# Kernel optimization log

Hardware: AMD Instinct MI355X
Metric: run time of the kernel (lower is better)

Reference implementation:

```python
import jax, jax.numpy as jnp
import numpy as np
import math

EMBED_DIM = 1024
MEMORY_DIM = 1024
MEMORY_SIZE = 2048
B, S = 8, 4096


def bitnet_linear(x, W, b):
    """Eval-mode BitNetLinear: 1.58-bit weight quant + 8-bit activation quant."""
    w_scale = jnp.mean(jnp.abs(W))
    qW = jnp.sign(W) * (jnp.abs(W) > 0.5 * w_scale).astype(W.dtype)
    i_scale = jnp.max(jnp.abs(x)) / 127.0
    qx = jnp.clip(jnp.round(x / i_scale), -128.0, 127.0)
    out = jnp.einsum('bsi,oi->bso', qx, qW) * (w_scale * i_scale)
    return out + b


def setup_inputs() -> dict:
    key = jax.random.key(0)
    ks = jax.random.split(key, 9)
    return {
        'x': jax.random.normal(ks[0], (B, S, EMBED_DIM), jnp.float32),
        'memory_keys': jax.random.normal(ks[1], (MEMORY_SIZE, MEMORY_DIM), jnp.float32),
        'memory_values': jax.random.normal(ks[2], (MEMORY_SIZE, EMBED_DIM), jnp.float32),
        'Wk': jax.random.normal(ks[3], (MEMORY_DIM, EMBED_DIM), jnp.float32) * 0.1,
        'bk': jnp.zeros((MEMORY_DIM,), jnp.float32),
        'Wv': jax.random.normal(ks[4], (EMBED_DIM, EMBED_DIM), jnp.float32) * 0.1,
        'bv': jnp.zeros((EMBED_DIM,), jnp.float32),
        'Wo': jax.random.normal(ks[5], (EMBED_DIM, EMBED_DIM), jnp.float32) * 0.1,
        'bo': jnp.zeros((EMBED_DIM,), jnp.float32),
    }


def reference(x, memory_keys, memory_values, Wk, bk, Wv, bv, Wo, bo):
    # quantized key/value projections
    query_keys = bitnet_linear(x, Wk, bk)          # [B, S, Dm]
    _query_values = bitnet_linear(x, Wv, bv)       # computed in original (used only by update path)
    # memory cross-attention over fixed bank
    similarities = jnp.einsum('bsd,md->bsm', query_keys, memory_keys)  # [B, S, M]
    attention_weights = jax.nn.softmax(similarities / math.sqrt(MEMORY_DIM), axis=-1)
    retrieved = jnp.einsum('bsm,me->bse', attention_weights, memory_values)  # [B, S, E]
    output = bitnet_linear(x + retrieved, Wo, bo)
    return output
```

## Files before the change

### kernel.cpp

```cpp
#include <hip/hip_runtime.h>
#include <hip/hip_bf16.h>
#include <stdint.h>
#include <type_traits>

typedef __attribute__((ext_vector_type(8))) short bf16x8;
typedef __attribute__((ext_vector_type(4))) int i32x4;
typedef __attribute__((ext_vector_type(16))) float f32x16;
typedef __attribute__((ext_vector_type(16))) int i32x16;

struct Scalars {
  double sum_wk;
  double sum_wo;
  unsigned int max_x_bits;
  unsigned int max_y_bits;
};

__device__ __forceinline__ unsigned short f2bf(float f) {
  __hip_bfloat16 h = __float2bfloat16(f);
  return *reinterpret_cast<unsigned short*>(&h);
}

__device__ __forceinline__ void async16(void* lds, const void* g) {
  __builtin_amdgcn_global_load_lds((__attribute__((address_space(1))) void*)g,
                                   (__attribute__((address_space(3))) void*)lds, 16, 0, 0);
}

__device__ __forceinline__ void tile_swizzle(int nxShift, int& bx, int& by) {
  const int per = gridDim.x >> 3;
  const int tile = (blockIdx.x & 7) * per + (blockIdx.x >> 3);
  bx = tile & ((1 << nxShift) - 1);
  by = tile >> nxShift;
}

__device__ __forceinline__ f32x16 mm32(bf16x8 a, bf16x8 b, f32x16 c) {
  return __builtin_amdgcn_mfma_f32_32x32x16_bf16(a, b, c, 0, 0, 0);
}
__device__ __forceinline__ i32x16 mm32(i32x4 a, i32x4 b, i32x16 c) {
  return __builtin_amdgcn_mfma_i32_32x32x32_i8(a, b, c, 0, 0, 0);
}

__global__ __launch_bounds__(256) void stats_kernel(const float* __restrict__ Wk,
                                                    const float* __restrict__ Wo,
                                                    const float* __restrict__ x,
                                                    Scalars* __restrict__ sc) {
  const int which = blockIdx.y;
  size_t tid = (size_t)blockIdx.x * 256 + threadIdx.x;
  size_t stride = (size_t)gridDim.x * 256;
  if (which < 2) {
    const float* w = which ? Wo : Wk;
    const size_t n = 1048576;
    double s = 0.0;
    for (size_t i = tid * 4; i < n; i += stride * 4) {
      float4 v = *(const float4*)(w + i);
      s += (double)fabsf(v.x) + (double)fabsf(v.y) + (double)fabsf(v.z) + (double)fabsf(v.w);
    }
#pragma unroll
    for (int o = 32; o > 0; o >>= 1) s += __shfl_xor(s, o);
    __shared__ double sm[4];
    if ((threadIdx.x & 63) == 0) sm[threadIdx.x >> 6] = s;
    __syncthreads();
    if (threadIdx.x == 0)
      atomicAdd(which ? &sc->sum_wo : &sc->sum_wk, sm[0] + sm[1] + sm[2] + sm[3]);
  } else {
    const size_t n = (size_t)32768 * 1024;
    float m = 0.0f;
    for (size_t i = tid * 4; i < n; i += stride * 4) {
      float4 v = *(const float4*)(x + i);
      m = fmaxf(m, fmaxf(fmaxf(fabsf(v.x), fabsf(v.y)), fmaxf(fabsf(v.z), fabsf(v.w))));
    }
#pragma unroll
    for (int o = 32; o > 0; o >>= 1) m = fmaxf(m, __shfl_xor(m, o));
    __shared__ float smf[4];
    if ((threadIdx.x & 63) == 0) smf[threadIdx.x >> 6] = m;
    __syncthreads();
    if (threadIdx.x == 0)
      atomicMax(&sc->max_x_bits,
                __float_as_uint(fmaxf(fmaxf(smf[0], smf[1]), fmaxf(smf[2], smf[3]))));
  }
}

__global__ __launch_bounds__(256) void prep_kernel(
    const float* __restrict__ Wk, const float* __restrict__ Wo,
    const float* __restrict__ mk, const float* __restrict__ mv,
    const float* __restrict__ x, char* __restrict__ qWk8, char* __restrict__ qWo8,
    __hip_bfloat16* __restrict__ mkb, __hip_bfloat16* __restrict__ mvT,
    char* __restrict__ qx8, const Scalars* __restrict__ sc) {
  __shared__ float tl[32][33];
  const int which = blockIdx.y;
  const int t = threadIdx.x;
  size_t tid = (size_t)blockIdx.x * 256 + t;
  size_t stride = (size_t)gridDim.x * 256;
  if (which < 2) {
    const float* W = which ? Wo : Wk;
    char* q = which ? qWo8 : qWk8;
    const double sum = which ? sc->sum_wo : sc->sum_wk;
    const float thr = 0.5f * (float)(sum * (1.0 / 1048576.0));
    const size_t n = 1048576;
    for (size_t i = tid * 4; i < n; i += stride * 4) {
      float4 v = *(const float4*)(W + i);
      char4 o;
      o.x = (char)(fabsf(v.x) > thr ? (v.x > 0.f ? 1 : -1) : 0);
      o.y = (char)(fabsf(v.y) > thr ? (v.y > 0.f ? 1 : -1) : 0);
      o.z = (char)(fabsf(v.z) > thr ? (v.z > 0.f ? 1 : -1) : 0);
      o.w = (char)(fabsf(v.w) > thr ? (v.w > 0.f ? 1 : -1) : 0);
      *(char4*)(q + i) = o;
    }
  } else if (which == 2) {
    const size_t n = (size_t)2048 * 1024;
    for (size_t i = tid * 4; i < n; i += stride * 4) {
      float4 v = *(const float4*)(mk + i);
      ushort4 o;
      o.x = f2bf(v.x); o.y = f2bf(v.y); o.z = f2bf(v.z); o.w = f2bf(v.w);
      *(ushort4*)((unsigned short*)mkb + i) = o;
    }
  } else if (which == 3) {
    const int ti = blockIdx.x & 31;
    const int tj = blockIdx.x >> 5;
    const int tx = t & 31, ty = t >> 5;
#pragma unroll
    for (int r = 0; r < 4; ++r)
      tl[ty + r * 8][tx] = mv[(size_t)(tj * 32 + ty + r * 8) * 1024 + ti * 32 + tx];
    __syncthreads();
#pragma unroll
    for (int r = 0; r < 4; ++r)
      mvT[(size_t)(ti * 32 + ty + r * 8) * 2048 + tj * 32 + tx] =
          __float2bfloat16(tl[tx][ty + r * 8]);
  } else {
    const float isc = __uint_as_float(sc->max_x_bits) / 127.0f;
    const size_t n = (size_t)32768 * 1024;
    for (size_t i = tid * 4; i < n; i += stride * 4) {
      float4 v = *(const float4*)(x + i);
      char4 o;
      o.x = (char)(int)fminf(fmaxf(rintf(v.x / isc), -128.f), 127.f);
      o.y = (char)(int)fminf(fmaxf(rintf(v.y / isc), -128.f), 127.f);
      o.z = (char)(int)fminf(fmaxf(rintf(v.z / isc), -128.f), 127.f);
      o.w = (char)(int)fminf(fmaxf(rintf(v.w / isc), -128.f), 127.f);
      *(char4*)(qx8 + i) = o;
    }
  }
}

__global__ __launch_bounds__(256) void quant_act_i8_kernel(const float* __restrict__ x,
                                                           char* __restrict__ q,
                                                           const unsigned int* __restrict__ maxbits,
                                                           size_t n) {
  const float isc = __uint_as_float(*maxbits) / 127.0f;
  size_t tid = (size_t)blockIdx.x * blockDim.x + threadIdx.x;
  size_t stride = (size_t)gridDim.x * blockDim.x;
  for (size_t i = tid * 4; i < n; i += stride * 4) {
    float4 v = *(const float4*)(x + i);
    char4 o;
    o.x = (char)(int)fminf(fmaxf(rintf(v.x / isc), -128.f), 127.f);
    o.y = (char)(int)fminf(fmaxf(rintf(v.y / isc), -128.f), 127.f);
    o.z = (char)(int)fminf(fmaxf(rintf(v.z / isc), -128.f), 127.f);
    o.w = (char)(int)fminf(fmaxf(rintf(v.w / isc), -128.f), 127.f);
    *(char4*)(q + i) = o;
  }
}

__global__ __launch_bounds__(256) void softmax_kernel(__hip_bfloat16* __restrict__ sims) {
  unsigned short* row = (unsigned short*)(sims + (size_t)blockIdx.x * 2048);
  const int t = threadIdx.x;
  const int l = t & 63, wv = t >> 6;
  uint4 r4 = *(const uint4*)(row + t * 8);
  float v[8];
  v[0] = __uint_as_float(r4.x << 16); v[1] = __uint_as_float(r4.x & 0xffff0000u);
  v[2] = __uint_as_float(r4.y << 16); v[3] = __uint_as_float(r4.y & 0xffff0000u);
  v[4] = __uint_as_float(r4.z << 16); v[5] = __uint_as_float(r4.z & 0xffff0000u);
  v[6] = __uint_as_float(r4.w << 16); v[7] = __uint_as_float(r4.w & 0xffff0000u);
  float m = v[0];
#pragma unroll
  for (int i = 1; i < 8; ++i) m = fmaxf(m, v[i]);
#pragma unroll
  for (int o = 32; o > 0; o >>= 1) m = fmaxf(m, __shfl_xor(m, o));
  __shared__ float red[4], red2[4];
  if (l == 0) red[wv] = m;
  __syncthreads();
  m = fmaxf(fmaxf(red[0], red[1]), fmaxf(red[2], red[3]));
  float s = 0.f;
#pragma unroll
  for (int i = 0; i < 8; ++i) { v[i] = expf(v[i] - m); s += v[i]; }
#pragma unroll
  for (int o = 32; o > 0; o >>= 1) s += __shfl_xor(s, o);
  if (l == 0) red2[wv] = s;
  __syncthreads();
  s = red2[0] + red2[1] + red2[2] + red2[3];
  unsigned short b[8];
#pragma unroll
  for (int i = 0; i < 8; ++i) b[i] = f2bf(v[i] / s);
  uint4 o4;
  o4.x = (unsigned)b[0] | ((unsigned)b[1] << 16);
  o4.y = (unsigned)b[2] | ((unsigned)b[3] << 16);
  o4.z = (unsigned)b[4] | ((unsigned)b[5] << 16);
  o4.w = (unsigned)b[6] | ((unsigned)b[7] << 16);
  *(uint4*)(row + t * 8) = o4;
}

#define CFENCE() asm volatile("" ::: "memory")
#define BAR8() { CFENCE(); __builtin_amdgcn_s_barrier(); CFENCE(); }
#define WLGKM(N) { asm volatile("s_waitcnt lgkmcnt(" #N ")" ::: "memory"); __builtin_amdgcn_sched_barrier(0); }
#define WVM(N) asm volatile("s_waitcnt vmcnt(" #N ")" ::: "memory")

template <int EPI>
__global__ __launch_bounds__(512, 2) void gemm8(
    const char* __restrict__ A, const char* __restrict__ B, void* __restrict__ C,
    const float* __restrict__ aux, Scalars* __restrict__ sc,
    int Ndim, int KB, int nxShift) {
  constexpr bool I8 = (EPI >= 3);
  using FR  = typename std::conditional<I8, i32x4, bf16x8>::type;
  using ACC = typename std::conditional<I8, i32x16, f32x16>::type;
  __shared__ __align__(16) char lds[4][2][16384];

  int bx, by;
  tile_swizzle(nxShift, bx, by);
  const int rowBlk = by * 256, colBlk = bx * 256;

  const int t = threadIdx.x, w = t >> 6, l = t & 63;
  const int wm = w >> 2, wn = w & 3;
  const int l31 = l & 31, hi = l >> 5;
  const int NT = KB >> 7, NIT = NT >> 1;

  int voA[2][2], voB[2][2];
#pragma unroll
  for (int hf = 0; hf < 2; ++hf)
#pragma unroll
    for (int j = 0; j < 2; ++j) {
      const int idx = j * 64 + (t >> 3);
      const int kby = ((t & 7) ^ (idx & 7)) << 4;
      voA[hf][j] = (rowBlk + ((idx >> 6) << 7) + (hf << 6) + (idx & 63)) * KB + kby;
      voB[hf][j] = (colBlk + ((idx >> 5) << 6) + (hf << 5) + (idx & 31)) * KB + kby;
    }

  int ofsK[4];
#pragma unroll
  for (int ks = 0; ks < 4; ++ks)
    ofsK[ks] = ((((ks ^ ((l >> 1) & 3)) << 1) | (hi ^ (l & 1))) << 4);
  const char* bA = &lds[0][0][0] + (wm * 64 + l31) * 128;
  const char* bB = &lds[2][0][0] + (wn * 32 + l31) * 128;

#define STG_A(slot, hf, tk)                                                         \
  if ((tk) < NT) {                                                                  \
    _Pragma("unroll") for (int j = 0; j < 2; ++j)                                   \
      async16(&lds[hf][slot][j * 8192 + (w << 10)],                                 \
              A + (((size_t)(tk)) << 7) + voA[hf][j]);                              \
  }
#define STG_B(slot, hf, tk)                                                         \
  if ((tk) < NT) {                                                                  \
    _Pragma("unroll") for (int j = 0; j < 2; ++j)                                   \
      async16(&lds[2 + (hf)][slot][j * 8192 + (w << 10)],                           \
              B + (((size_t)(tk)) << 7) + voB[hf][j]);                              \
  }

#define LD_A(dst, slot, hf, f01, ks) \
  dst = *(const FR*)(bA + ((hf) * 32768 + (slot) * 16384 + (f01) * 4096) + ofsK[ks]);
#define LD_B(dst, slot, nh, ks) \
  dst = *(const FR*)(bB + ((nh) * 32768 + (slot) * 16384) + ofsK[ks]);

#define R_A0(s) { _Pragma("unroll") for (int f_ = 0; f_ < 2; ++f_) _Pragma("unroll") for (int k_ = 0; k_ < 4; ++k_) LD_A(af[f_][k_], s, 0, f_, k_); }
#define R_A1(s) { _Pragma("unroll") for (int f_ = 0; f_ < 2; ++f_) _Pragma("unroll") for (int k_ = 0; k_ < 4; ++k_) LD_A(af[f_][k_], s, 1, f_, k_); }
#define R_B0(s) { _Pragma("unroll") for (int k_ = 0; k_ < 4; ++k_) LD_B(b0[k_], s, 0, k_); }
#define R_B1(s) { _Pragma("unroll") for (int k_ = 0; k_ < 4; ++k_) LD_B(b1[k_], s, 1, k_); }

#define MM32(MH, NH, BR)                                                            \
  __builtin_amdgcn_s_setprio(1);                                                    \
  _Pragma("unroll") for (int k_ = 0; k_ < 4; ++k_)                                  \
    _Pragma("unroll") for (int f_ = 0; f_ < 2; ++f_)                                \
      acc[(MH) * 2 + f_][NH] = mm32(af[f_][k_], BR[k_], acc[(MH) * 2 + f_][NH]);    \
  __builtin_amdgcn_s_setprio(0);

#define TSTEP(s, tk, last)                                                          \
  {                                                                                 \
                     \
    R_B1(s);                                                                        \
    STG_A((s) ^ 1, 1, (tk) + 1);                                                    \
    BAR8(); WLGKM(4);                                                               \
    MM32(0, 0, b0);                                                                 \
    BAR8();                                                                         \
        \
    STG_A(s, 0, (tk) + 2);                                                          \
    BAR8(); WLGKM(0);                                                               \
    MM32(0, 1, b1);                                                                 \
    R_A1(s);                                                                        \
    BAR8();                                                                         \
                                                                \
    STG_B(s, 0, (tk) + 2);                                                          \
    BAR8(); WLGKM(0);                                                               \
    MM32(1, 0, b0);                                                                 \
    BAR8();                                                                         \
           \
    STG_B(s, 1, (tk) + 2);                                                          \
    if (last) { WVM(0); } else { WVM(6); }                                          \
    BAR8();                                                                         \
    MM32(1, 1, b1);                                                                 \
    R_A0((s) ^ 1); R_B0((s) ^ 1);                                                   \
  }

  FR af[2][4], b0[4], b1[4];
  ACC acc[4][2] = {};

  STG_A(0, 0, 0); STG_B(0, 0, 0); STG_B(0, 1, 0); STG_A(0, 1, 0);
  CFENCE();
  STG_A(1, 0, 1); STG_B(1, 0, 1); STG_B(1, 1, 1);
  WVM(6);
  BAR8();
  R_A0(0); R_B0(0);

  for (int it = 0; it < NIT; ++it) {
    const bool last = (it == NIT - 1);
    TSTEP(0, it * 2, last);
    TSTEP(1, it * 2 + 1, last);
  }

  float sK = 0.0f;
  if constexpr (EPI == 3)
    sK = (float)(sc->sum_wk * (1.0 / 1048576.0)) * (__uint_as_float(sc->max_x_bits) / 127.0f);
  if constexpr (EPI == 4)
    sK = (float)(sc->sum_wo * (1.0 / 1048576.0)) * (__uint_as_float(sc->max_y_bits) / 127.0f);

  float amax = 0.0f;
#pragma unroll
  for (int f = 0; f < 4; ++f) {
#pragma unroll
    for (int g = 0; g < 2; ++g) {
      const int col = colBlk + wn * 64 + g * 32 + l31;
#pragma unroll
      for (int r = 0; r < 16; ++r) {
        const int row = rowBlk + wm * 128 + f * 32 + (r & 3) + 8 * (r >> 2) + 4 * hi;
        if constexpr (EPI == 1) {
          ((__hip_bfloat16*)C)[(size_t)row * Ndim + col] =
              __float2bfloat16(acc[f][g][r] * 0.03125f);
        } else if constexpr (EPI == 2) {
          float v = acc[f][g][r] + aux[(size_t)row * Ndim + col];
          ((float*)C)[(size_t)row * Ndim + col] = v;
          amax = fmaxf(amax, fabsf(v));
        } else if constexpr (EPI == 3) {
          ((__hip_bfloat16*)C)[(size_t)row * Ndim + col] =
              __float2bfloat16((float)acc[f][g][r] * sK + aux[col]);
        } else {
          ((float*)C)[(size_t)row * Ndim + col] = (float)acc[f][g][r] * sK + aux[col];
        }
      }
    }
  }

  if constexpr (EPI == 2) {
    __shared__ float wred[8];
#pragma unroll
    for (int o = 32; o > 0; o >>= 1) amax = fmaxf(amax, __shfl_xor(amax, o));
    if (l == 0) wred[w] = amax;
    __syncthreads();
    if (t == 0) {
      float m = wred[0];
#pragma unroll
      for (int i = 1; i < 8; ++i) m = fmaxf(m, wred[i]);
      atomicMax(&sc->max_y_bits, __float_as_uint(m));
    }
  }
#undef STG_A
#undef STG_B
#undef LD_A
#undef LD_B
#undef R_A0
#undef R_A1
#undef R_B0
#undef R_B1
#undef MM32
#undef TSTEP
}

extern "C" void kernel_launch(void* const* d_in, const int* in_sizes, int n_in,
                              void* d_out, int out_size, void* d_ws, size_t ws_size,
                              hipStream_t stream) {
  (void)in_sizes; (void)n_in; (void)out_size; (void)ws_size;
  const float* x  = (const float*)d_in[0];
  const float* mk = (const float*)d_in[1];
  const float* mv = (const float*)d_in[2];
  const float* Wk = (const float*)d_in[3];
  const float* bk = (const float*)d_in[4];
  const float* Wo = (const float*)d_in[7];
  const float* bo = (const float*)d_in[8];
  float* out = (float*)d_out;

  const int M = 32768, E = 1024, MEM = 2048;

  char* ws = (char*)d_ws;
  Scalars* sc = (Scalars*)ws;
  const size_t off0 = 256;
  char* qx8 = ws + off0;
  __hip_bfloat16* qk = (__hip_bfloat16*)(ws + off0 + (size_t)M * E);
  float* y = (float*)(ws + off0);
  const size_t off1 = off0 + (size_t)M * E * 4;
  __hip_bfloat16* sims = (__hip_bfloat16*)(ws + off1);
  char* qy8 = (char*)sims;
  const size_t off2 = off1 + (size_t)M * MEM * 2;
  char* qWk8 = ws + off2;
  char* qWo8 = qWk8 + (size_t)E * E;
  __hip_bfloat16* mkb = (__hip_bfloat16*)(qWo8 + (size_t)E * E);
  __hip_bfloat16* mvT = mkb + (size_t)MEM * E;

  hipMemsetAsync(ws, 0, 256, stream);

  stats_kernel<<<dim3(1024, 3), dim3(256), 0, stream>>>(Wk, Wo, x, sc);
  prep_kernel<<<dim3(2048, 5), dim3(256), 0, stream>>>(Wk, Wo, mk, mv, x, qWk8, qWo8,
                                                       mkb, mvT, qx8, sc);

  gemm8<3><<<dim3((E / 256) * (M / 256)), dim3(512), 0, stream>>>(
      qx8, qWk8, qk, bk, sc, E, E, 2);
  gemm8<1><<<dim3((MEM / 256) * (M / 256)), dim3(512), 0, stream>>>(
      (const char*)qk, (const char*)mkb, sims, nullptr, sc, MEM, 2 * E, 3);
  softmax_kernel<<<dim3(M), dim3(256), 0, stream>>>(sims);
  gemm8<2><<<dim3((E / 256) * (M / 256)), dim3(512), 0, stream>>>(
      (const char*)sims, (const char*)mvT, y, x, sc, E, 2 * MEM, 2);
  quant_act_i8_kernel<<<dim3(2048), dim3(256), 0, stream>>>(y, qy8, &sc->max_y_bits, (size_t)M * E);
  gemm8<4><<<dim3((E / 256) * (M / 256)), dim3(512), 0, stream>>>(
      qy8, qWo8, out, bo, sc, E, E, 2);
}
```

Baseline: 738.0 us.

## Switch GEMM inner loop from 32x32 to 16x16 MFMA tiles

Replaces the 32x32x16 bf16 and 32x32x32 i8 MFMA instructions with the 16x16x32 bf16 and 16x16x64 i8 variants. The LDS fragment addressing, the swizzle, the register fragment layout and the epilogue row/column mapping are all rebuilt for 16x16 tiles. The explicit lgkmcnt waits are removed, so the compiler now inserts the LDS waits. The per-block amax reduction through shared memory is replaced by one atomicMax per wave. This risks different LDS read patterns and scheduling, and makes more atomics per block.

```diff
diff --git a/kernel.cpp b/kernel.cpp
--- a/kernel.cpp
+++ b/kernel.cpp
@@ -4,9 +4,8 @@
 #include <type_traits>
 
 typedef __attribute__((ext_vector_type(8))) short bf16x8;
+typedef __attribute__((ext_vector_type(4))) float f32x4;
 typedef __attribute__((ext_vector_type(4))) int i32x4;
-typedef __attribute__((ext_vector_type(16))) float f32x16;
-typedef __attribute__((ext_vector_type(16))) int i32x16;
 
 struct Scalars {
   double sum_wk;
@@ -32,11 +31,11 @@
   by = tile >> nxShift;
 }
 
-__device__ __forceinline__ f32x16 mm32(bf16x8 a, bf16x8 b, f32x16 c) {
-  return __builtin_amdgcn_mfma_f32_32x32x16_bf16(a, b, c, 0, 0, 0);
-}
-__device__ __forceinline__ i32x16 mm32(i32x4 a, i32x4 b, i32x16 c) {
-  return __builtin_amdgcn_mfma_i32_32x32x32_i8(a, b, c, 0, 0, 0);
+__device__ __forceinline__ f32x4 mm(bf16x8 a, bf16x8 b, f32x4 c) {
+  return __builtin_amdgcn_mfma_f32_16x16x32_bf16(a, b, c, 0, 0, 0);
+}
+__device__ __forceinline__ i32x4 mm(i32x4 a, i32x4 b, i32x4 c) {
+  return __builtin_amdgcn_mfma_i32_16x16x64_i8(a, b, c, 0, 0, 0);
 }
 
 __global__ __launch_bounds__(256) void stats_kernel(const float* __restrict__ Wk,
@@ -198,7 +197,6 @@
 
 #define CFENCE() asm volatile("" ::: "memory")
 #define BAR8() { CFENCE(); __builtin_amdgcn_s_barrier(); CFENCE(); }
-#define WLGKM(N) { asm volatile("s_waitcnt lgkmcnt(" #N ")" ::: "memory"); __builtin_amdgcn_sched_barrier(0); }
 #define WVM(N) asm volatile("s_waitcnt vmcnt(" #N ")" ::: "memory")
 
 template <int EPI>
@@ -208,7 +206,7 @@
     int Ndim, int KB, int nxShift) {
   constexpr bool I8 = (EPI >= 3);
   using FR  = typename std::conditional<I8, i32x4, bf16x8>::type;
-  using ACC = typename std::conditional<I8, i32x16, f32x16>::type;
+  using ACC = typename std::conditional<I8, i32x4, f32x4>::type;
   __shared__ __align__(16) char lds[4][2][16384];
 
   int bx, by;
@@ -217,7 +215,7 @@
 
   const int t = threadIdx.x, w = t >> 6, l = t & 63;
   const int wm = w >> 2, wn = w & 3;
-  const int l31 = l & 31, hi = l >> 5;
+  const int quad = l >> 4, m16 = l & 15;
   const int NT = KB >> 7, NIT = NT >> 1;
 
   int voA[2][2], voB[2][2];
@@ -231,12 +229,14 @@
       voB[hf][j] = (colBlk + ((idx >> 5) << 6) + (hf << 5) + (idx & 31)) * KB + kby;
     }
 
-  int ofsK[4];
-#pragma unroll
-  for (int ks = 0; ks < 4; ++ks)
-    ofsK[ks] = ((((ks ^ ((l >> 1) & 3)) << 1) | (hi ^ (l & 1))) << 4);
-  const char* bA = &lds[0][0][0] + (wm * 64 + l31) * 128;
-  const char* bB = &lds[2][0][0] + (wn * 32 + l31) * 128;
+  const char* baA[2];
+  const char* baB[2];
+#pragma unroll
+  for (int ks = 0; ks < 2; ++ks) {
+    const int x16 = ((ks << 6) + (quad << 4)) ^ ((m16 & 7) << 4);
+    baA[ks] = &lds[0][0][(wm * 64 + m16) * 128 + x16];
+    baB[ks] = &lds[2][0][(wn * 32 + m16) * 128 + x16];
+  }
 
 #define STG_A(slot, hf, tk)                                                         \
   if ((tk) < NT) {                                                                  \
@@ -251,52 +251,55 @@
               B + (((size_t)(tk)) << 7) + voB[hf][j]);                              \
   }
 
-#define LD_A(dst, slot, hf, f01, ks) \
-  dst = *(const FR*)(bA + ((hf) * 32768 + (slot) * 16384 + (f01) * 4096) + ofsK[ks]);
-#define LD_B(dst, slot, nh, ks) \
-  dst = *(const FR*)(bB + ((nh) * 32768 + (slot) * 16384) + ofsK[ks]);
-
-#define R_A0(s) { _Pragma("unroll") for (int f_ = 0; f_ < 2; ++f_) _Pragma("unroll") for (int k_ = 0; k_ < 4; ++k_) LD_A(af[f_][k_], s, 0, f_, k_); }
-#define R_A1(s) { _Pragma("unroll") for (int f_ = 0; f_ < 2; ++f_) _Pragma("unroll") for (int k_ = 0; k_ < 4; ++k_) LD_A(af[f_][k_], s, 1, f_, k_); }
-#define R_B0(s) { _Pragma("unroll") for (int k_ = 0; k_ < 4; ++k_) LD_B(b0[k_], s, 0, k_); }
-#define R_B1(s) { _Pragma("unroll") for (int k_ = 0; k_ < 4; ++k_) LD_B(b1[k_], s, 1, k_); }
-
-#define MM32(MH, NH, BR)                                                            \
+#define LD_A(dst, slot, hf, f, ks) \
+  dst = *(const FR*)(baA[ks] + ((hf)*32768 + (slot)*16384 + (f)*2048));
+#define LD_B(dst, slot, hf, gg, ks) \
+  dst = *(const FR*)(baB[ks] + ((hf)*32768 + (slot)*16384 + (gg)*2048));
+
+#define R_A0(s) { _Pragma("unroll") for (int f_ = 0; f_ < 4; ++f_) { LD_A(af[f_][0], s, 0, f_, 0); LD_A(af[f_][1], s, 0, f_, 1); } }
+#define R_A1(s) { _Pragma("unroll") for (int f_ = 0; f_ < 4; ++f_) { LD_A(af[f_][0], s, 1, f_, 0); LD_A(af[f_][1], s, 1, f_, 1); } }
+#define R_B0(s) { _Pragma("unroll") for (int g_ = 0; g_ < 2; ++g_) { LD_B(b0[g_][0], s, 0, g_, 0); LD_B(b0[g_][1], s, 0, g_, 1); } }
+#define R_B1(s) { _Pragma("unroll") for (int g_ = 0; g_ < 2; ++g_) { LD_B(b1[g_][0], s, 1, g_, 0); LD_B(b1[g_][1], s, 1, g_, 1); } }
+
+#define MM8(FO, GO, BR)                                                             \
   __builtin_amdgcn_s_setprio(1);                                                    \
-  _Pragma("unroll") for (int k_ = 0; k_ < 4; ++k_)                                  \
-    _Pragma("unroll") for (int f_ = 0; f_ < 2; ++f_)                                \
-      acc[(MH) * 2 + f_][NH] = mm32(af[f_][k_], BR[k_], acc[(MH) * 2 + f_][NH]);    \
+  _Pragma("unroll") for (int f_ = 0; f_ < 4; ++f_)                                  \
+    _Pragma("unroll") for (int g_ = 0; g_ < 2; ++g_) {                              \
+      acc[(FO) + f_][(GO) + g_] = mm(af[f_][0], BR[g_][0], acc[(FO) + f_][(GO) + g_]); \
+      acc[(FO) + f_][(GO) + g_] = mm(af[f_][1], BR[g_][1], acc[(FO) + f_][(GO) + g_]); \
+    }                                                                               \
   __builtin_amdgcn_s_setprio(0);
 
 #define TSTEP(s, tk, last)                                                          \
   {                                                                                 \
-                     \
+                                         \
     R_B1(s);                                                                        \
     STG_A((s) ^ 1, 1, (tk) + 1);                                                    \
-    BAR8(); WLGKM(4);                                                               \
-    MM32(0, 0, b0);                                                                 \
+    BAR8();                                                                         \
+    MM8(0, 0, b0);                                                                  \
     BAR8();                                                                         \
         \
     STG_A(s, 0, (tk) + 2);                                                          \
-    BAR8(); WLGKM(0);                                                               \
-    MM32(0, 1, b1);                                                                 \
+    BAR8();                                                                         \
+    MM8(0, 2, b1);                                                                  \
     R_A1(s);                                                                        \
     BAR8();                                                                         \
                                                                 \
     STG_B(s, 0, (tk) + 2);                                                          \
-    BAR8(); WLGKM(0);                                                               \
-    MM32(1, 0, b0);                                                                 \
+    BAR8();                                                                         \
+    MM8(4, 0, b0);                                                                  \
     BAR8();                                                                         \
            \
     STG_B(s, 1, (tk) + 2);                                                          \
     if (last) { WVM(0); } else { WVM(6); }                                          \
     BAR8();                                                                         \
-    MM32(1, 1, b1);                                                                 \
-    R_A0((s) ^ 1); R_B0((s) ^ 1);                                                   \
-  }
-
-  FR af[2][4], b0[4], b1[4];
-  ACC acc[4][2] = {};
+    MM8(4, 2, b1);                                                                  \
+    R_A0((s) ^ 1);                                                                  \
+    R_B0((s) ^ 1);                                                                  \
+  }
+
+  FR af[4][2], b0[2][2], b1[2][2];
+  ACC acc[8][4] = {};
 
   STG_A(0, 0, 0); STG_B(0, 0, 0); STG_B(0, 1, 0); STG_A(0, 1, 0);
   CFENCE();
@@ -319,42 +322,34 @@
 
   float amax = 0.0f;
 #pragma unroll
-  for (int f = 0; f < 4; ++f) {
-#pragma unroll
-    for (int g = 0; g < 2; ++g) {
-      const int col = colBlk + wn * 64 + g * 32 + l31;
-#pragma unroll
-      for (int r = 0; r < 16; ++r) {
-        const int row = rowBlk + wm * 128 + f * 32 + (r & 3) + 8 * (r >> 2) + 4 * hi;
+  for (int f = 0; f < 8; ++f) {
+#pragma unroll
+    for (int g = 0; g < 4; ++g) {
+      const int col = colBlk + wn * 64 + g * 16 + m16;
+#pragma unroll
+      for (int rg = 0; rg < 4; ++rg) {
+        const int row = rowBlk + wm * 128 + f * 16 + quad * 4 + rg;
         if constexpr (EPI == 1) {
           ((__hip_bfloat16*)C)[(size_t)row * Ndim + col] =
-              __float2bfloat16(acc[f][g][r] * 0.03125f);
+              __float2bfloat16(acc[f][g][rg] * 0.03125f);
         } else if constexpr (EPI == 2) {
-          float v = acc[f][g][r] + aux[(size_t)row * Ndim + col];
+          float v = acc[f][g][rg] + aux[(size_t)row * Ndim + col];
           ((float*)C)[(size_t)row * Ndim + col] = v;
           amax = fmaxf(amax, fabsf(v));
         } else if constexpr (EPI == 3) {
           ((__hip_bfloat16*)C)[(size_t)row * Ndim + col] =
-              __float2bfloat16((float)acc[f][g][r] * sK + aux[col]);
+              __float2bfloat16((float)acc[f][g][rg] * sK + aux[col]);
         } else {
-          ((float*)C)[(size_t)row * Ndim + col] = (float)acc[f][g][r] * sK + aux[col];
+          ((float*)C)[(size_t)row * Ndim + col] = (float)acc[f][g][rg] * sK + aux[col];
         }
       }
     }
   }
 
   if constexpr (EPI == 2) {
-    __shared__ float wred[8];
 #pragma unroll
     for (int o = 32; o > 0; o >>= 1) amax = fmaxf(amax, __shfl_xor(amax, o));
-    if (l == 0) wred[w] = amax;
-    __syncthreads();
-    if (t == 0) {
-      float m = wred[0];
-#pragma unroll
-      for (int i = 1; i < 8; ++i) m = fmaxf(m, wred[i]);
-      atomicMax(&sc->max_y_bits, __float_as_uint(m));
-    }
+    if (l == 0) atomicMax(&sc->max_y_bits, __float_as_uint(amax));
   }
 #undef STG_A
 #undef STG_B
@@ -364,7 +359,7 @@
 #undef R_A1
 #undef R_B0
 #undef R_B1
-#undef MM32
+#undef MM8
 #undef TSTEP
 }
 
```

After: 755.9 us. 2.4% more time.
